# Performance work log

Measured on AMD Instinct MI355X. Metric: run time of the kernel, lower is better.

## Reference

```python
import jax, jax.numpy as jnp
import numpy as np

T_STEPS = 32      # discrete samples along each pixel's voting ray
RAY_STEP = 4.0    # pixel stride between ray samples


def setup_inputs() -> dict:
    key = jax.random.key(0)
    k1, k2, k3, k4 = jax.random.split(key, 4)
    B, C, H, W = 2, 22, 480, 640
    label = jax.random.randint(k1, (B, H, W), 0, C, dtype=jnp.int32)
    vertex = jax.random.normal(k2, (B, 3 * C, H, W), dtype=jnp.float32)
    # per-class 3D extents in meters (~0..0.3 m objects)
    extents = jax.random.uniform(k3, (C, 3), dtype=jnp.float32) * 0.3
    # flattened intrinsics [fx, 0, cx, 0, fy, cy, 0, 0, 1]
    intr = jnp.array([572.4, 0.0, 325.3, 0.0, 573.6, 242.0, 0.0, 0.0, 1.0], dtype=jnp.float32)
    meta_data = jnp.tile(intr[None, :], (B, 1))
    gt = jax.random.normal(k4, (B, C, 4, 4), dtype=jnp.float32)
    return {"label": label, "vertex": vertex, "extents": extents,
            "meta_data": meta_data, "gt": gt, "is_train": 0}


def reference(label, vertex, extents, meta_data, gt, is_train):
    B, C3, H, W = vertex.shape
    C = C3 // 3
    HW = H * W
    f32 = jnp.float32

    # Gather each pixel's class-specific vertex prediction: (nx, ny, z)
    v = vertex.reshape(B, C, 3, HW)                        # (B,C,3,HW)
    lab = label.reshape(B, HW)                             # (B,HW) int
    idx = jnp.broadcast_to(lab[:, None, None, :], (B, 1, 3, HW))
    g = jnp.take_along_axis(v, idx, axis=1)[:, 0]          # (B,3,HW)
    nx, ny, z = g[:, 0], g[:, 1], g[:, 2]
    inv_norm = 1.0 / (jnp.sqrt(nx * nx + ny * ny) + 1e-8)
    nx = nx * inv_norm
    ny = ny * inv_norm

    # Pixel coordinates
    pix = jnp.arange(HW, dtype=jnp.int32)
    xs = (pix % W).astype(f32)
    ys = (pix // W).astype(f32)

    # Cast T_STEPS votes along the predicted ray toward the object center
    t = (jnp.arange(1, T_STEPS + 1, dtype=f32) * RAY_STEP)  # (T,)
    px = jnp.round(xs[None, :, None] + nx[:, :, None] * t[None, None, :]).astype(jnp.int32)
    py = jnp.round(ys[None, :, None] + ny[:, :, None] * t[None, None, :]).astype(jnp.int32)
    inb = (px >= 0) & (px < W) & (py >= 0) & (py < H)
    fg = (lab > 0)[:, :, None]                              # background casts no votes
    w = (inb & fg).astype(f32)                              # (B,HW,T)
    flat = jnp.clip(py, 0, H - 1) * W + jnp.clip(px, 0, W - 1)

    # Scatter-accumulate votes into per-class Hough space (B,C,HW)
    b_idx = jnp.arange(B)[:, None, None]
    acc = jnp.zeros((B, C, HW), dtype=f32).at[b_idx, lab[:, :, None], flat].add(w)

    # Peak detection: argmax per (batch, class)
    peak = jnp.argmax(acc, axis=-1)                         # (B,C)
    votes = jnp.max(acc, axis=-1)                           # (B,C)
    cx = (peak % W).astype(f32)
    cy = (peak // W).astype(f32)

    # Mean predicted depth per class (masked mean over that class's pixels)
    b2 = jnp.arange(B)[:, None]
    cnt = jnp.zeros((B, C), dtype=f32).at[b2, lab].add(1.0)
    zsum = jnp.zeros((B, C), dtype=f32).at[b2, lab].add(z)
    depth = zsum / jnp.maximum(cnt, 1.0)

    # Project object extents to image-plane box size: half = 0.5*|extent|*fx/depth
    fx = meta_data[:, 0][:, None]                           # (B,1)
    diag = jnp.linalg.norm(extents, axis=-1)[None, :]       # (1,C)
    half = 0.5 * diag * fx / jnp.maximum(jnp.abs(depth), 1e-3)

    cls = jnp.broadcast_to(jnp.arange(C, dtype=f32)[None, :], (B, C))
    out = jnp.stack([cls, votes,
                     cx - half, cy - half, cx + half, cy + half,
                     cx, cy, depth], axis=-1)               # (B,C,9)
    return out
```

## Files before the change

kernel.cpp:

```cpp
#include <hip/hip_runtime.h>


#define MAXC 32
#define NSEG 4

__global__ __launch_bounds__(512) void emit_kernel(
    const int* __restrict__ label, const float* __restrict__ vertex,
    unsigned short* __restrict__ bucketData, unsigned* __restrict__ cursor,
    unsigned* __restrict__ cnt, float* __restrict__ zsum,
    int C, int H, int W, int HW, int SEGCAP, int NB)
{
    __shared__ unsigned s_bin[512];
    __shared__ unsigned s_rel[512];
    __shared__ unsigned s_gb[512];
    __shared__ unsigned s_ccnt[MAXC];
    __shared__ float s_cz[MAXC];

    int tid = threadIdx.x;
    int b = blockIdx.y;
    int p = blockIdx.x * 512 + tid;
    int seg = blockIdx.x & (NSEG - 1);

    s_bin[tid] = 0u;
    s_rel[tid] = 0u;
    if (tid < MAXC) { s_ccnt[tid] = 0u; s_cz[tid] = 0.0f; }
    __syncthreads();

    int lab = 0;
    bool fg = false;
    float nxn = 0.f, nyn = 0.f, xs = 0.f, ys = 0.f;
    if (p < HW) {
        lab = label[(size_t)b * HW + p];
        const float* vb = vertex + ((size_t)(b * 3 * C + 3 * lab)) * HW + p;
        float nx = vb[0];
        float ny = vb[(size_t)HW];
        float z  = vb[2 * (size_t)HW];
        atomicAdd(&s_ccnt[lab], 1u);
        atomicAdd(&s_cz[lab], z);
        if (lab > 0) {
            fg = true;
            float nrm = __fsqrt_rn(__fadd_rn(__fmul_rn(nx, nx), __fmul_rn(ny, ny)));
            float inv = __fdiv_rn(1.0f, __fadd_rn(nrm, 1e-8f));
            nxn = __fmul_rn(nx, inv);
            nyn = __fmul_rn(ny, inv);
            xs = (float)(p % W);
            ys = (float)(p / W);
        }
    }

    if (fg) {
        #pragma unroll
        for (int i = 1; i <= 32; ++i) {
            float t = (float)i * 4.0f;
            int px = (int)rintf(__fadd_rn(xs, __fmul_rn(nxn, t)));
            int py = (int)rintf(__fadd_rn(ys, __fmul_rn(nyn, t)));
            if (px >= 0 && px < W && py >= 0 && py < H)
                atomicAdd(&s_bin[py], 1u);
        }
    }
    __syncthreads();

    if (tid < H) {
        unsigned n = s_bin[tid];
        s_gb[tid] = n ? atomicAdd(&cursor[seg * NB + b * H + tid], n) : 0u;
    }
    __syncthreads();

    if (fg) {
        unsigned labsh = (unsigned)lab << 10;
        #pragma unroll
        for (int i = 1; i <= 32; ++i) {
            float t = (float)i * 4.0f;
            int px = (int)rintf(__fadd_rn(xs, __fmul_rn(nxn, t)));
            int py = (int)rintf(__fadd_rn(ys, __fmul_rn(nyn, t)));
            if (px >= 0 && px < W && py >= 0 && py < H) {
                unsigned rel = atomicAdd(&s_rel[py], 1u);
                unsigned g = s_gb[py] + rel;
                if (g < (unsigned)SEGCAP)
                    bucketData[((size_t)(b * H + py) * NSEG + seg) * SEGCAP + g] =
                        (unsigned short)(labsh | (unsigned)px);
            }
        }
    }

    if (tid < C) {
        unsigned c = s_ccnt[tid];
        if (c) {
            atomicAdd(&cnt[b * C + tid], c);
            atomicAdd(&zsum[b * C + tid], s_cz[tid]);
        }
    }
}

__global__ __launch_bounds__(256) void hist_kernel(
    const unsigned short* __restrict__ bucketData,
    const unsigned* __restrict__ cursor,
    unsigned long long* __restrict__ keys,
    int C, int H, int W, int SEGCAP, int NB)
{
    extern __shared__ char sm[];
    unsigned* hist = (unsigned*)sm;
    unsigned long long* s_wb =
        (unsigned long long*)(sm + (size_t)(C * W / 2) * 4);

    int tid = threadIdx.x;
    int lane = tid & 63, wave = tid >> 6;
    int py = blockIdx.x;
    int b = blockIdx.y;
    int words = C * W / 2;

    for (int i = tid; i < words; i += 256) hist[i] = 0u;
    __syncthreads();

    int bucket = b * H + py;
    #pragma unroll
    for (int seg = 0; seg < NSEG; ++seg) {
        unsigned n = cursor[seg * NB + bucket];
        if (n > (unsigned)SEGCAP) n = (unsigned)SEGCAP;
        const unsigned short* src =
            bucketData + ((size_t)bucket * NSEG + seg) * SEGCAP;
        for (unsigned i = tid; i < n; i += 256) {
            unsigned r = src[i];
            unsigned idx = (r >> 10) * (unsigned)W + (r & 1023u);
            atomicAdd(&hist[idx >> 1], 1u << ((idx & 1u) * 16));
        }
    }
    __syncthreads();

    unsigned rowbase = (unsigned)py * (unsigned)W;
    for (int c = 0; c < C; ++c) {
        unsigned long long best = 0;
        for (int px = tid; px < W; px += 256) {
            unsigned cv = (hist[(unsigned)(c * W + px) >> 1] >> ((px & 1) * 16)) & 0xFFFFu;
            unsigned long long k = ((unsigned long long)cv << 32)
                                 | (unsigned long long)(0xFFFFFFFFu - (rowbase + px));
            if (k > best) best = k;
        }
        #pragma unroll
        for (int off = 32; off > 0; off >>= 1) {
            unsigned long long o = __shfl_xor(best, off, 64);
            if (o > best) best = o;
        }
        if (lane == 0) s_wb[c * 4 + wave] = best;
    }
    __syncthreads();
    if (tid < C) {
        unsigned long long m = s_wb[tid * 4];
        #pragma unroll
        for (int w2 = 1; w2 < 4; ++w2)
            if (s_wb[tid * 4 + w2] > m) m = s_wb[tid * 4 + w2];
        atomicMax(&keys[b * C + tid], m);
    }
}

__global__ void finalize_kernel(const unsigned long long* __restrict__ keys,
                                const unsigned* __restrict__ cnt,
                                const float* __restrict__ zsum,
                                const float* __restrict__ extents,
                                const float* __restrict__ meta,
                                float* __restrict__ out,
                                int B, int C, int W)
{
    int i = threadIdx.x;
    if (i >= B * C) return;
    int b = i / C, c = i % C;
    unsigned long long k = keys[i];
    unsigned votes = (unsigned)(k >> 32);
    unsigned peak = 0xFFFFFFFFu - (unsigned)(k & 0xFFFFFFFFull);
    float cx = (float)(peak % (unsigned)W);
    float cy = (float)(peak / (unsigned)W);
    float n = (float)cnt[i];
    float depth = zsum[i] / fmaxf(n, 1.0f);
    float fx = meta[b * 9 + 0];
    const float* e = extents + c * 3;
    float diag = sqrtf(e[0] * e[0] + e[1] * e[1] + e[2] * e[2]);
    float half = 0.5f * diag * fx / fmaxf(fabsf(depth), 0.001f);
    float* o = out + (size_t)i * 9;
    o[0] = (float)c;
    o[1] = (float)votes;
    o[2] = cx - half;
    o[3] = cy - half;
    o[4] = cx + half;
    o[5] = cy + half;
    o[6] = cx;
    o[7] = cy;
    o[8] = depth;
}

extern "C" void kernel_launch(void* const* d_in, const int* in_sizes, int n_in,
                              void* d_out, int out_size, void* d_ws, size_t ws_size,
                              hipStream_t stream)
{
    const int* label    = (const int*)d_in[0];
    const float* vertex = (const float*)d_in[1];
    const float* extents= (const float*)d_in[2];
    const float* meta   = (const float*)d_in[3];

    int C = in_sizes[2] / 3;
    int B = in_sizes[3] / 9;
    int HW = in_sizes[0] / B;
    const int W = 640;
    int H = HW / W;
    int NB = B * H;

    size_t keysOff = 0;
    size_t curOff  = keysOff + (size_t)B * C * 8;
    size_t cntOff  = curOff + (size_t)NSEG * NB * 4;
    size_t zsumOff = cntOff + (size_t)B * C * 4;
    size_t zeroEnd = zsumOff + (size_t)B * C * 4;
    size_t dataOff = (zeroEnd + 63) & ~(size_t)63;

    size_t availRec = (ws_size > dataOff) ? (ws_size - dataOff) / ((size_t)NB * NSEG * 2) : 0;
    int SEGCAP = (int)(availRec > 8192 ? 8192 : availRec);
    SEGCAP &= ~63;

    unsigned long long* keys = (unsigned long long*)((char*)d_ws + keysOff);
    unsigned* cursor         = (unsigned*)((char*)d_ws + curOff);
    unsigned* cnt            = (unsigned*)((char*)d_ws + cntOff);
    float* zsum              = (float*)((char*)d_ws + zsumOff);
    unsigned short* bucketData = (unsigned short*)((char*)d_ws + dataOff);

    hipMemsetAsync(d_ws, 0, zeroEnd, stream);

    dim3 egrid((HW + 511) / 512, B);
    emit_kernel<<<egrid, 512, 0, stream>>>(label, vertex, bucketData, cursor,
                                           cnt, zsum, C, H, W, HW, SEGCAP, NB);

    dim3 hgrid(H, B);
    size_t hsm = (size_t)(C * W / 2) * 4 + (size_t)C * 4 * 8;
    hist_kernel<<<hgrid, 256, hsm, stream>>>(bucketData, cursor, keys, C, H, W, SEGCAP, NB);

    finalize_kernel<<<1, 64, 0, stream>>>(keys, cnt, zsum, extents, meta,
                                          (float*)d_out, B, C, W);
}
```

Before: 121.2 us.

## Replace global cursor atomics with per-block scanned vote chunks and partial sums

The emit kernel now exclusive-scans its per-row vote counts in shared memory. It writes votes into a private per-block chunk and records a (offset,count) table, instead of reserving space through global atomic cursors into per-row segments. Per-class count and depth sums are written as per-block partials and reduced in a widened finalize kernel, so only the keys still need a memset. The hist kernel walks the table, with each thread serially reading one block's run for its row. That removes global atomic contention and the segment-capacity clamp, but it makes the hist loads per-thread serial and less coalesced.

```diff
diff --git a/kernel.cpp b/kernel.cpp
--- a/kernel.cpp
+++ b/kernel.cpp
@@ -2,27 +2,25 @@
 
 
 #define MAXC 32
-#define NSEG 4
 
 __global__ __launch_bounds__(512) void emit_kernel(
     const int* __restrict__ label, const float* __restrict__ vertex,
-    unsigned short* __restrict__ bucketData, unsigned* __restrict__ cursor,
-    unsigned* __restrict__ cnt, float* __restrict__ zsum,
-    int C, int H, int W, int HW, int SEGCAP, int NB)
+    unsigned short* __restrict__ chunk, unsigned* __restrict__ table,
+    unsigned* __restrict__ cntPart, float* __restrict__ zsumPart,
+    int C, int H, int W, int HW, int GX)
 {
     __shared__ unsigned s_bin[512];
-    __shared__ unsigned s_rel[512];
-    __shared__ unsigned s_gb[512];
+    __shared__ unsigned s_pos[512];
+    __shared__ unsigned s_wtot[8];
     __shared__ unsigned s_ccnt[MAXC];
     __shared__ float s_cz[MAXC];
 
     int tid = threadIdx.x;
-    int b = blockIdx.y;
-    int p = blockIdx.x * 512 + tid;
-    int seg = blockIdx.x & (NSEG - 1);
+    int lane = tid & 63, wave = tid >> 6;
+    int b = blockIdx.y, g = blockIdx.x;
+    int p = g * 512 + tid;
 
     s_bin[tid] = 0u;
-    s_rel[tid] = 0u;
     if (tid < MAXC) { s_ccnt[tid] = 0u; s_cz[tid] = 0.0f; }
     __syncthreads();
 
@@ -60,43 +58,52 @@
     }
     __syncthreads();
 
-    if (tid < H) {
-        unsigned n = s_bin[tid];
-        s_gb[tid] = n ? atomicAdd(&cursor[seg * NB + b * H + tid], n) : 0u;
-    }
+    unsigned own = s_bin[tid];
+    unsigned v = own;
+    #pragma unroll
+    for (int off = 1; off < 64; off <<= 1) {
+        unsigned u = __shfl_up(v, off, 64);
+        if (lane >= off) v += u;
+    }
+    if (lane == 63) s_wtot[wave] = v;
+    __syncthreads();
+    if (tid == 0) {
+        unsigned a = 0;
+        #pragma unroll
+        for (int w2 = 0; w2 < 8; ++w2) { unsigned t2 = s_wtot[w2]; s_wtot[w2] = a; a += t2; }
+    }
+    __syncthreads();
+    unsigned base = v + s_wtot[wave] - own;
+    s_pos[tid] = base;
+    table[((size_t)b * GX + g) * 512 + tid] = (base << 16) | own;
     __syncthreads();
 
     if (fg) {
         unsigned labsh = (unsigned)lab << 10;
+        unsigned short* myChunk = chunk + (((size_t)b * GX + g) << 14);
         #pragma unroll
         for (int i = 1; i <= 32; ++i) {
             float t = (float)i * 4.0f;
             int px = (int)rintf(__fadd_rn(xs, __fmul_rn(nxn, t)));
             int py = (int)rintf(__fadd_rn(ys, __fmul_rn(nyn, t)));
             if (px >= 0 && px < W && py >= 0 && py < H) {
-                unsigned rel = atomicAdd(&s_rel[py], 1u);
-                unsigned g = s_gb[py] + rel;
-                if (g < (unsigned)SEGCAP)
-                    bucketData[((size_t)(b * H + py) * NSEG + seg) * SEGCAP + g] =
-                        (unsigned short)(labsh | (unsigned)px);
+                unsigned slot = atomicAdd(&s_pos[py], 1u);
+                myChunk[slot] = (unsigned short)(labsh | (unsigned)px);
             }
         }
     }
 
     if (tid < C) {
-        unsigned c = s_ccnt[tid];
-        if (c) {
-            atomicAdd(&cnt[b * C + tid], c);
-            atomicAdd(&zsum[b * C + tid], s_cz[tid]);
-        }
+        cntPart[((size_t)b * GX + g) * MAXC + tid] = s_ccnt[tid];
+        zsumPart[((size_t)b * GX + g) * MAXC + tid] = s_cz[tid];
     }
 }
 
 __global__ __launch_bounds__(256) void hist_kernel(
-    const unsigned short* __restrict__ bucketData,
-    const unsigned* __restrict__ cursor,
+    const unsigned short* __restrict__ chunk,
+    const unsigned* __restrict__ table,
     unsigned long long* __restrict__ keys,
-    int C, int H, int W, int SEGCAP, int NB)
+    int C, int H, int W, int GX)
 {
     extern __shared__ char sm[];
     unsigned* hist = (unsigned*)sm;
@@ -112,14 +119,12 @@
     for (int i = tid; i < words; i += 256) hist[i] = 0u;
     __syncthreads();
 
-    int bucket = b * H + py;
-    #pragma unroll
-    for (int seg = 0; seg < NSEG; ++seg) {
-        unsigned n = cursor[seg * NB + bucket];
-        if (n > (unsigned)SEGCAP) n = (unsigned)SEGCAP;
-        const unsigned short* src =
-            bucketData + ((size_t)bucket * NSEG + seg) * SEGCAP;
-        for (unsigned i = tid; i < n; i += 256) {
+    for (int g = tid; g < GX; g += 256) {
+        unsigned e = table[((size_t)b * GX + g) * 512 + py];
+        unsigned n = e & 0xFFFFu;
+        if (!n) continue;
+        const unsigned short* src = chunk + (((size_t)b * GX + g) << 14) + (e >> 16);
+        for (unsigned i = 0; i < n; ++i) {
             unsigned r = src[i];
             unsigned idx = (r >> 10) * (unsigned)W + (r & 1023u);
             atomicAdd(&hist[idx >> 1], 1u << ((idx & 1u) * 16));
@@ -153,38 +158,63 @@
     }
 }
 
-__global__ void finalize_kernel(const unsigned long long* __restrict__ keys,
-                                const unsigned* __restrict__ cnt,
-                                const float* __restrict__ zsum,
-                                const float* __restrict__ extents,
-                                const float* __restrict__ meta,
-                                float* __restrict__ out,
-                                int B, int C, int W)
-{
-    int i = threadIdx.x;
-    if (i >= B * C) return;
-    int b = i / C, c = i % C;
-    unsigned long long k = keys[i];
-    unsigned votes = (unsigned)(k >> 32);
-    unsigned peak = 0xFFFFFFFFu - (unsigned)(k & 0xFFFFFFFFull);
-    float cx = (float)(peak % (unsigned)W);
-    float cy = (float)(peak / (unsigned)W);
-    float n = (float)cnt[i];
-    float depth = zsum[i] / fmaxf(n, 1.0f);
-    float fx = meta[b * 9 + 0];
-    const float* e = extents + c * 3;
-    float diag = sqrtf(e[0] * e[0] + e[1] * e[1] + e[2] * e[2]);
-    float half = 0.5f * diag * fx / fmaxf(fabsf(depth), 0.001f);
-    float* o = out + (size_t)i * 9;
-    o[0] = (float)c;
-    o[1] = (float)votes;
-    o[2] = cx - half;
-    o[3] = cy - half;
-    o[4] = cx + half;
-    o[5] = cy + half;
-    o[6] = cx;
-    o[7] = cy;
-    o[8] = depth;
+__global__ __launch_bounds__(512) void finalize_kernel(
+    const unsigned long long* __restrict__ keys,
+    const unsigned* __restrict__ cntPart,
+    const float* __restrict__ zsumPart,
+    const float* __restrict__ extents,
+    const float* __restrict__ meta,
+    float* __restrict__ out,
+    int B, int C, int W, int GX)
+{
+    __shared__ float s_cnt[64];
+    __shared__ float s_z[64];
+
+    int tid = threadIdx.x;
+    int lane = tid & 63, wave = tid >> 6;
+    int P = B * C;
+
+    for (int pair = wave; pair < P; pair += 8) {
+        int b = pair / C, c = pair % C;
+        unsigned cs = 0; float zs = 0.f;
+        for (int g = lane; g < GX; g += 64) {
+            size_t idx = ((size_t)b * GX + g) * MAXC + c;
+            cs += cntPart[idx];
+            zs += zsumPart[idx];
+        }
+        #pragma unroll
+        for (int off = 32; off > 0; off >>= 1) {
+            cs += __shfl_xor(cs, off, 64);
+            zs += __shfl_xor(zs, off, 64);
+        }
+        if (lane == 0) { s_cnt[pair] = (float)cs; s_z[pair] = zs; }
+    }
+    __syncthreads();
+
+    if (tid < P) {
+        int b = tid / C, c = tid % C;
+        unsigned long long k = keys[tid];
+        unsigned votes = (unsigned)(k >> 32);
+        unsigned peak = 0xFFFFFFFFu - (unsigned)(k & 0xFFFFFFFFull);
+        float cx = (float)(peak % (unsigned)W);
+        float cy = (float)(peak / (unsigned)W);
+        float n = s_cnt[tid];
+        float depth = s_z[tid] / fmaxf(n, 1.0f);
+        float fx = meta[b * 9 + 0];
+        const float* e = extents + c * 3;
+        float diag = sqrtf(e[0] * e[0] + e[1] * e[1] + e[2] * e[2]);
+        float half = 0.5f * diag * fx / fmaxf(fabsf(depth), 0.001f);
+        float* o = out + (size_t)tid * 9;
+        o[0] = (float)c;
+        o[1] = (float)votes;
+        o[2] = cx - half;
+        o[3] = cy - half;
+        o[4] = cx + half;
+        o[5] = cy + half;
+        o[6] = cx;
+        o[7] = cy;
+        o[8] = depth;
+    }
 }
 
 extern "C" void kernel_launch(void* const* d_in, const int* in_sizes, int n_in,
@@ -201,35 +231,33 @@
     int HW = in_sizes[0] / B;
     const int W = 640;
     int H = HW / W;
-    int NB = B * H;
-
-    size_t keysOff = 0;
-    size_t curOff  = keysOff + (size_t)B * C * 8;
-    size_t cntOff  = curOff + (size_t)NSEG * NB * 4;
-    size_t zsumOff = cntOff + (size_t)B * C * 4;
-    size_t zeroEnd = zsumOff + (size_t)B * C * 4;
-    size_t dataOff = (zeroEnd + 63) & ~(size_t)63;
-
-    size_t availRec = (ws_size > dataOff) ? (ws_size - dataOff) / ((size_t)NB * NSEG * 2) : 0;
-    int SEGCAP = (int)(availRec > 8192 ? 8192 : availRec);
-    SEGCAP &= ~63;
+    int GX = (HW + 511) / 512;
+
+    size_t keysOff  = 0;
+    size_t keysBytes= (size_t)B * C * 8;
+    size_t cpOff    = (keysBytes + 63) & ~(size_t)63;
+    size_t cpBytes  = (size_t)B * GX * MAXC * 4;
+    size_t zpOff    = cpOff + cpBytes;
+    size_t tabOff   = zpOff + cpBytes;
+    size_t tabBytes = (size_t)B * GX * 512 * 4;
+    size_t chOff    = (tabOff + tabBytes + 63) & ~(size_t)63;
 
     unsigned long long* keys = (unsigned long long*)((char*)d_ws + keysOff);
-    unsigned* cursor         = (unsigned*)((char*)d_ws + curOff);
-    unsigned* cnt            = (unsigned*)((char*)d_ws + cntOff);
-    float* zsum              = (float*)((char*)d_ws + zsumOff);
-    unsigned short* bucketData = (unsigned short*)((char*)d_ws + dataOff);
-
-    hipMemsetAsync(d_ws, 0, zeroEnd, stream);
-
-    dim3 egrid((HW + 511) / 512, B);
-    emit_kernel<<<egrid, 512, 0, stream>>>(label, vertex, bucketData, cursor,
-                                           cnt, zsum, C, H, W, HW, SEGCAP, NB);
+    unsigned* cntPart        = (unsigned*)((char*)d_ws + cpOff);
+    float* zsumPart          = (float*)((char*)d_ws + zpOff);
+    unsigned* table          = (unsigned*)((char*)d_ws + tabOff);
+    unsigned short* chunk    = (unsigned short*)((char*)d_ws + chOff);
+
+    hipMemsetAsync(d_ws, 0, keysBytes, stream);
+
+    dim3 egrid(GX, B);
+    emit_kernel<<<egrid, 512, 0, stream>>>(label, vertex, chunk, table,
+                                           cntPart, zsumPart, C, H, W, HW, GX);
 
     dim3 hgrid(H, B);
     size_t hsm = (size_t)(C * W / 2) * 4 + (size_t)C * 4 * 8;
-    hist_kernel<<<hgrid, 256, hsm, stream>>>(bucketData, cursor, keys, C, H, W, SEGCAP, NB);
-
-    finalize_kernel<<<1, 64, 0, stream>>>(keys, cnt, zsum, extents, meta,
-                                          (float*)d_out, B, C, W);
-}
+    hist_kernel<<<hgrid, 256, hsm, stream>>>(chunk, table, keys, C, H, W, GX);
+
+    finalize_kernel<<<1, 512, 0, stream>>>(keys, cntPart, zsumPart, extents,
+                                           meta, (float*)d_out, B, C, W, GX);
+}
```

New measurement: 148.0 us. 1.22x slower.
